# Kernel optimization log

Hardware: AMD Instinct MI355X
Metric: run time of the kernel (lower is better)

The kernel has to match this reference:

```python
import jax, jax.numpy as jnp
import numpy as np

B, T, C = 64, 512, 1024
D = C // 2  # split_len1 == split_len2
CLAMP = 5.0


def e(s):
    # exp(clamp * 0.636 * atan(s / clamp))
    return jnp.exp(CLAMP * 0.636 * jnp.arctan(s / CLAMP))


def gru_cell(x, h, Wih, Whh, bih, bhh):
    # Standard GRU cell, gate order (r, z, n) as in torch.nn.GRUCell.
    gi = x @ Wih.T + bih  # [B, 3D]
    gh = h @ Whh.T + bhh  # [B, 3D]
    i_r, i_z, i_n = gi[:, :D], gi[:, D:2 * D], gi[:, 2 * D:]
    h_r, h_z, h_n = gh[:, :D], gh[:, D:2 * D], gh[:, 2 * D:]
    r = jax.nn.sigmoid(i_r + h_r)
    z = jax.nn.sigmoid(i_z + h_z)
    n = jnp.tanh(i_n + r * h_n)
    return (1.0 - z) * n + z * h


def setup_inputs() -> dict:
    key = jax.random.key(0)
    ks = jax.random.split(key, 20)

    def p(k, shape, scale=0.05):
        return jax.random.normal(k, shape, jnp.float32) * scale

    inp = {"x": jax.random.normal(ks[0], (B, T, C), jnp.float32)}
    for i, name in enumerate(["s1", "s2"]):
        b = 1 + i * 6
        inp[f"{name}_Wih"] = p(ks[b], (3 * D, D))
        inp[f"{name}_Whh"] = p(ks[b + 1], (3 * D, D))
        inp[f"{name}_bih"] = p(ks[b + 2], (3 * D,))
        inp[f"{name}_bhh"] = p(ks[b + 3], (3 * D,))
        inp[f"{name}_Wo"] = p(ks[b + 4], (2 * D, D))
        inp[f"{name}_bo"] = p(ks[b + 5], (2 * D,))
    inp["cg1_W"] = p(ks[13], (D, D))
    inp["cg1_b"] = p(ks[14], (D,))
    inp["cg2_W"] = p(ks[15], (D, D))
    inp["cg2_b"] = p(ks[16], (D,))
    return inp


def reference(x, s1_Wih, s1_Whh, s1_bih, s1_bhh, s1_Wo, s1_bo,
              s2_Wih, s2_Whh, s2_bih, s2_bhh, s2_Wo, s2_bo,
              cg1_W, cg1_b, cg2_W, cg2_b):
    batch = x.shape[0]

    def step(carry, xt):
        h1, h2 = carry
        x1, x2 = xt[:, :D], xt[:, D:]
        # s2 GRU block on x2
        h2n = gru_cell(x2, h2, s2_Wih, s2_Whh, s2_bih, s2_bhh)
        r2 = h2n @ s2_Wo.T + s2_bo
        s2v, t2 = r2[:, :D], r2[:, D:]
        y1 = e(s2v) * x1 + t2
        # gate x2 with cg1 of OLD h1
        x2g = x2 * e(h1 @ cg1_W.T + cg1_b)
        # s1 GRU block on y1
        h1n = gru_cell(y1, h1, s1_Wih, s1_Whh, s1_bih, s1_bhh)
        r1 = h1n @ s1_Wo.T + s1_bo
        s1v, t1 = r1[:, :D], r1[:, D:]
        y2 = e(s1v) * x2g + t1
        # gate y1 with cg2 of OLD h2
        y1o = y1 * e(h2 @ cg2_W.T + cg2_b)
        return (h1n, h2n), jnp.concatenate([y1o, y2], axis=1)

    h0 = (jnp.zeros((batch, D), x.dtype), jnp.zeros((batch, D), x.dtype))
    _, ys = jax.lax.scan(step, h0, jnp.swapaxes(x, 0, 1))  # [T, B, C]
    return jnp.swapaxes(ys, 0, 1)  # [B, T, C]
```

## Files before the change

kernel.cpp:

```cpp
#include <hip/hip_runtime.h>
#include <math.h>

constexpr int kT = 512;
constexpr int kC = 1024;
constexpr int kD = 512;

typedef __attribute__((ext_vector_type(8))) short bf16x8;
typedef __attribute__((ext_vector_type(4))) float f32x4;
typedef __attribute__((ext_vector_type(4))) unsigned int u32x4;

__device__ __forceinline__ float b2f(unsigned short u) {
  unsigned int v = ((unsigned int)u) << 16;
  return __builtin_bit_cast(float, v);
}
__device__ __forceinline__ unsigned short f2b(float f) {
  unsigned int u = __builtin_bit_cast(unsigned int, f);
  u += 0x7fffu + ((u >> 16) & 1u);
  return (unsigned short)(u >> 16);
}
__device__ __forceinline__ float sigm(float x) {
  x = fminf(15.f, fmaxf(-15.f, x));
  return 1.f / (1.f + __expf(-x));
}
__device__ __forceinline__ float tanh_(float x) {
  x = fminf(15.f, fmaxf(-15.f, x));
  float e2 = __expf(2.f * x);
  return (e2 - 1.f) / (e2 + 1.f);
}
__device__ __forceinline__ float efun(float s) {
  return __expf((5.0f * 0.636f) * atanf(s * 0.2f));
}

__device__ __forceinline__ void st_b16_wt(unsigned short* p, unsigned short v) {
  asm volatile("global_store_short %0, %1, off sc0 sc1" ::"v"(p),
               "v"((unsigned int)v)
               : "memory");
}
__device__ __forceinline__ void st_f32_wt(float* p, float v) {
  asm volatile("global_store_dword %0, %1, off sc0 sc1" ::"v"(p), "v"(v)
               : "memory");
}

__device__ __forceinline__ unsigned int ldflag(const unsigned int* p) {
  return __hip_atomic_load(p, __ATOMIC_RELAXED, __HIP_MEMORY_SCOPE_AGENT);
}

__global__ __launch_bounds__(256) void cvt_x2_kernel(
    const float* __restrict__ x, unsigned short* __restrict__ xb2) {
  const int idx = blockIdx.x * 256 + threadIdx.x;
  const int e = idx * 8;
  const int dd = e & 511;
  const int tb = e >> 9;
  const int b = tb & 63;
  const int t = tb >> 6;
  const float* src = x + ((size_t)b * kT + t) * kC + kD + dd;
  f32x4 v0 = *(const f32x4*)src;
  f32x4 v1 = *(const f32x4*)(src + 4);
  bf16x8 o;
#pragma unroll
  for (int j = 0; j < 4; j++) {
    o[j] = (short)f2b(v0[j]);
    o[j + 4] = (short)f2b(v1[j]);
  }
  *(bf16x8*)(xb2 + e) = o;
}

__global__ __launch_bounds__(256, 1) void fused_glow_kernel(
    const float* __restrict__ x, const unsigned short* __restrict__ xb2,
    const float* __restrict__ A_Wih, const float* __restrict__ A_Whh,
    const float* __restrict__ A_bih, const float* __restrict__ A_bhh,
    const float* __restrict__ A_Wo, const float* __restrict__ A_bo,
    const float* __restrict__ A_cgW, const float* __restrict__ A_cgb,
    const float* __restrict__ B_Wih, const float* __restrict__ B_Whh,
    const float* __restrict__ B_bih, const float* __restrict__ B_bhh,
    const float* __restrict__ B_Wo, const float* __restrict__ B_bo,
    const float* __restrict__ B_cgW, const float* __restrict__ B_cgb,
    unsigned short* __restrict__ y1buf, float* __restrict__ out,
    unsigned short* __restrict__ hbA, unsigned short* __restrict__ hbB,
    unsigned int* __restrict__ flagsA, unsigned int* __restrict__ flagsB) {
  const int g = blockIdx.x;
  const bool isA = (g < 64);
  const int gl = isA ? g : (g - 64);
  const int tid = threadIdx.x;
  const int w = tid >> 6;
  const int l = tid & 63;
  const int q = l & 15;
  const int kg = l >> 4;
  const bool lo = (q < 8);
  const int qm = q & 7;
  const int d = 8 * gl + qm;
  const int browbase = 16 * w + 4 * kg;
  const int arow = 16 * w + q;
  const int acol = kg * 8;

  const float* Wih = isA ? A_Wih : B_Wih;
  const float* Whh = isA ? A_Whh : B_Whh;
  const float* bih = isA ? A_bih : B_bih;
  const float* bhh = isA ? A_bhh : B_bhh;
  const float* Wo = isA ? A_Wo : B_Wo;
  const float* bo = isA ? A_bo : B_bo;
  const float* cgW = isA ? A_cgW : B_cgW;
  const float* cgb = isA ? A_cgb : B_cgb;
  unsigned short* hbuf = isA ? hbA : hbB;
  unsigned int* myflag = (isA ? flagsA : flagsB) + (size_t)w * 64 + gl;
  const unsigned int* pollA = flagsA + (size_t)w * 64;
  const unsigned int* pollB = flagsB + (size_t)w * 64;

  __shared__ __attribute__((aligned(16))) unsigned short wlds[80 * 512];
  for (int c = tid; c < 80 * 64; c += 256) {
    const int u = c >> 6, kb = c & 63;
    const int s8 = 8 * gl + (u & 7);
    const int sel = u >> 3;
    u32x4 v = {0u, 0u, 0u, 0u};
    if (sel < 9) {
      const float* wrp = (sel == 0)   ? Whh + (size_t)s8 * kD
                         : (sel == 1) ? Whh + (size_t)(512 + s8) * kD
                         : (sel == 2) ? Whh + (size_t)(1024 + s8) * kD
                         : (sel == 3) ? cgW + (size_t)s8 * kD
                         : (sel == 4) ? Wo + (size_t)s8 * kD
                         : (sel == 5) ? Wo + (size_t)(512 + s8) * kD
                         : (sel == 6) ? Wih + (size_t)s8 * kD
                         : (sel == 7) ? Wih + (size_t)(512 + s8) * kD
                                      : Wih + (size_t)(1024 + s8) * kD;
      const float* p = wrp + kb * 8;
#pragma unroll
      for (int j = 0; j < 4; j++)
        v[j] = (unsigned int)f2b(p[2 * j]) | ((unsigned int)f2b(p[2 * j + 1]) << 16);
    }
    const int byteoff = u * 1024 + ((kb * 16) ^ ((u & 15) << 4));
    *(u32x4*)((char*)wlds + byteoff) = v;
  }

  float biasv[5];
  biasv[0] = lo ? bhh[d] : bhh[512 + d];
  biasv[1] = lo ? bhh[1024 + d] : cgb[d];
  biasv[2] = lo ? bo[d] : bo[512 + d];
  biasv[3] = lo ? bih[d] : bih[512 + d];
  biasv[4] = lo ? bih[1024 + d] : 0.f;

  float hsl[4] = {0.f, 0.f, 0.f, 0.f};
  float ecp[4];
#pragma unroll
  for (int r = 0; r < 4; r++) ecp[r] = efun(cgb[d]);

  __syncthreads();

  const int sw = q << 4;
  const int s0 = isA ? 0 : 2;
  const int s1 = isA ? 512 : 514;
#pragma unroll 1
  for (int s = s0; s <= s1; ++s) {
    const int it = isA ? s : (s - 2);

    bf16x8 ax[16];
    float xopf[4] = {0.f, 0.f, 0.f, 0.f};
    if (isA) {
      const int itc = it < 511 ? it : 511;
      const unsigned short* xp = xb2 + ((size_t)itc * 64 + arow) * 512 + acol;
#pragma unroll
      for (int kk = 0; kk < 16; kk++) ax[kk] = *(const bf16x8*)(xp + kk * 32);
      if (lo) {
        const int ttc = s >= 1 ? s - 1 : 0;
#pragma unroll
        for (int r = 0; r < 4; r++)
          xopf[r] = x[(size_t)(browbase + r) * (kT * kC) + (size_t)ttc * kC + d];
      }
      if (s >= 1) {
        const unsigned int* fp = pollA + l;
        unsigned int v = ldflag(fp);
        while (!__all((int)(v >= (unsigned)s))) {
          __builtin_amdgcn_s_sleep(1);
          v = ldflag(fp);
        }
      }
    } else {
      if (lo) {
        const int ttc = it >= 1 ? it - 1 : 0;
#pragma unroll
        for (int r = 0; r < 4; r++)
          xopf[r] =
              x[(size_t)(browbase + r) * (kT * kC) + (size_t)ttc * kC + kD + d];
      }
      {
        const unsigned int tgtA = (unsigned)(s <= 513 ? s : 513);
        const unsigned int* fp = pollA + l;
        unsigned int v = ldflag(fp);
        while (!__all((int)(v >= tgtA))) {
          __builtin_amdgcn_s_sleep(1);
          v = ldflag(fp);
        }
      }
      const int ity = it < 511 ? it : 511;
      const unsigned short* yp = y1buf + ((size_t)ity * 64 + arow) * 512 + acol;
#pragma unroll
      for (int kk = 0; kk < 16; kk++) ax[kk] = *(const bf16x8*)(yp + kk * 32);
      if (s >= 3) {
        const unsigned int* fp = pollB + l;
        unsigned int v = ldflag(fp);
        while (!__all((int)(v >= (unsigned)s))) {
          __builtin_amdgcn_s_sleep(1);
          v = ldflag(fp);
        }
      }
    }

    const unsigned short* hp =
        hbuf + (size_t)(isA ? s : it) * 32768 + (size_t)arow * 512 + acol;
    bf16x8 ah[16];
#pragma unroll
    for (int kk = 0; kk < 16; kk++) ah[kk] = *(const bf16x8*)(hp + kk * 32);

    f32x4 acc0 = {0.f, 0.f, 0.f, 0.f}, acc1 = {0.f, 0.f, 0.f, 0.f};
    f32x4 acc2 = {0.f, 0.f, 0.f, 0.f}, acc3 = {0.f, 0.f, 0.f, 0.f};
    f32x4 acc4 = {0.f, 0.f, 0.f, 0.f};
#pragma unroll
    for (int kk = 0; kk < 16; kk++) {
      const int kbyte = (kk * 32 + kg * 8) * 2;
      bf16x8 b0 = *(const bf16x8*)((const char*)wlds + q * 1024 + (kbyte ^ sw));
      bf16x8 b1 =
          *(const bf16x8*)((const char*)wlds + (16 + q) * 1024 + (kbyte ^ sw));
      bf16x8 b2 =
          *(const bf16x8*)((const char*)wlds + (32 + q) * 1024 + (kbyte ^ sw));
      bf16x8 b3 =
          *(const bf16x8*)((const char*)wlds + (48 + q) * 1024 + (kbyte ^ sw));
      bf16x8 b4 =
          *(const bf16x8*)((const char*)wlds + (64 + q) * 1024 + (kbyte ^ sw));
      acc0 = __builtin_amdgcn_mfma_f32_16x16x32_bf16(ah[kk], b0, acc0, 0, 0, 0);
      acc1 = __builtin_amdgcn_mfma_f32_16x16x32_bf16(ah[kk], b1, acc1, 0, 0, 0);
      acc2 = __builtin_amdgcn_mfma_f32_16x16x32_bf16(ah[kk], b2, acc2, 0, 0, 0);
      acc3 = __builtin_amdgcn_mfma_f32_16x16x32_bf16(ax[kk], b3, acc3, 0, 0, 0);
      acc4 = __builtin_amdgcn_mfma_f32_16x16x32_bf16(ax[kk], b4, acc4, 0, 0, 0);
    }
    float ab0[4], ab1[4], ab2[4], ab3[4], ab4[4];
#pragma unroll
    for (int r = 0; r < 4; r++) {
      ab0[r] = acc0[r] + biasv[0];
      ab1[r] = acc1[r] + biasv[1];
      ab2[r] = acc2[r] + biasv[2];
      ab3[r] = acc3[r] + biasv[3];
      ab4[r] = acc4[r] + biasv[4];
    }
    float ghz[4], tv[4], giz[4], ec_sh[4];
#pragma unroll
    for (int r = 0; r < 4; r++) {
      ghz[r] = __shfl_xor(ab0[r], 8, 64);
      tv[r] = __shfl_xor(ab2[r], 8, 64);
      giz[r] = __shfl_xor(ab3[r], 8, 64);
      ec_sh[r] = __shfl_xor(ecp[r], 8, 64);
    }

    const int tt = it - 1;
    float yvs[4] = {0.f, 0.f, 0.f, 0.f};
    if (lo) {
#pragma unroll
      for (int r = 0; r < 4; r++) {
        const int b = browbase + r;
        if (isA && it >= 1) {
          yvs[r] = efun(ab2[r]) * xopf[r] + tv[r];
          st_b16_wt(y1buf + ((size_t)tt * 64 + b) * 512 + d, f2b(yvs[r]));
        }
        if (it <= 511) {
          const float rr = sigm(ab3[r] + ab0[r]);
          const float zz = sigm(giz[r] + ghz[r]);
          const float nn = tanh_(ab4[r] + rr * ab1[r]);
          const float hn = (1.f - zz) * nn + zz * hsl[r];
          hsl[r] = hn;
          st_b16_wt(hbuf + (size_t)(it + 1) * 32768 + (size_t)b * 512 + d,
                    f2b(hn));
        }
      }
    } else {
#pragma unroll
      for (int r = 0; r < 4; r++) ecp[r] = efun(ab1[r]);
    }

    asm volatile("s_waitcnt vmcnt(0)" ::: "memory");
    if (l == 0)
      __hip_atomic_store(myflag, (unsigned)(s + 1), __ATOMIC_RELAXED,
                         __HIP_MEMORY_SCOPE_AGENT);

    if (lo && it >= 1) {
#pragma unroll
      for (int r = 0; r < 4; r++) {
        const int b = browbase + r;
        float* op =
            out + (size_t)b * (kT * kC) + (size_t)tt * kC + (isA ? 0 : kD) + d;
        if (isA) {
          st_f32_wt(op, yvs[r] * ec_sh[r]);
        } else {
          st_f32_wt(op, efun(ab2[r]) * (xopf[r] * ec_sh[r]) + tv[r]);
        }
      }
    }
  }
}

extern "C" void kernel_launch(void* const* d_in, const int* in_sizes, int n_in,
                              void* d_out, int out_size, void* d_ws, size_t ws_size,
                              hipStream_t stream) {
  (void)in_sizes; (void)n_in; (void)out_size; (void)ws_size;
  const float* x = (const float*)d_in[0];
  const float* s1_Wih = (const float*)d_in[1];
  const float* s1_Whh = (const float*)d_in[2];
  const float* s1_bih = (const float*)d_in[3];
  const float* s1_bhh = (const float*)d_in[4];
  const float* s1_Wo = (const float*)d_in[5];
  const float* s1_bo = (const float*)d_in[6];
  const float* s2_Wih = (const float*)d_in[7];
  const float* s2_Whh = (const float*)d_in[8];
  const float* s2_bih = (const float*)d_in[9];
  const float* s2_bhh = (const float*)d_in[10];
  const float* s2_Wo = (const float*)d_in[11];
  const float* s2_bo = (const float*)d_in[12];
  const float* cg1_W = (const float*)d_in[13];
  const float* cg1_b = (const float*)d_in[14];
  const float* cg2_W = (const float*)d_in[15];
  const float* cg2_b = (const float*)d_in[16];
  float* out = (float*)d_out;
  char* ws = (char*)d_ws;

  unsigned short* xb2 = (unsigned short*)ws;
  unsigned short* y1b = (unsigned short*)(ws + 33554432);
  unsigned short* hbA = (unsigned short*)(ws + 67108864);
  unsigned short* hbB = (unsigned short*)(ws + 100728832);
  unsigned int* flagsA = (unsigned int*)(ws + 134348800);
  unsigned int* flagsB = (unsigned int*)(ws + 134348800 + 4096);

  hipMemsetAsync(ws + 67108864, 0, 65536, stream);
  hipMemsetAsync(ws + 100728832, 0, 65536, stream);
  hipMemsetAsync(ws + 134348800, 0, 8192, stream);

  cvt_x2_kernel<<<8192, 256, 0, stream>>>(x, xb2);

  fused_glow_kernel<<<128, 256, 0, stream>>>(
      x, xb2,
      s2_Wih, s2_Whh, s2_bih, s2_bhh, s2_Wo, s2_bo, cg2_W, cg2_b,
      s1_Wih, s1_Whh, s1_bih, s1_bhh, s1_Wo, s1_bo, cg1_W, cg1_b,
      y1b, out, hbA, hbB, flagsA, flagsB);
}
```

Measured before the change: 3.664 ms.

## Co-locate both GRU chains in one 512-thread block per column slice

The A and B recurrent chains now share a single 512-thread workgroup per 8-column slice, so the grid drops from 128 to 64 blocks. Both weight sets are staged together in a larger LDS buffer of 144 rows, and the fifth weight tile is trimmed to 8 live rows with its own swizzle instead of zero padding. Cross-chain data can then be exchanged on the same CU, and fewer CUs take part in the global flag spin-waits. In exchange each block uses twice the LDS and threads, and both chains now compete for one CU's MFMA and memory bandwidth.

```diff
diff --git a/kernel.cpp b/kernel.cpp
--- a/kernel.cpp
+++ b/kernel.cpp
@@ -65,7 +65,7 @@
   *(bf16x8*)(xb2 + e) = o;
 }
 
-__global__ __launch_bounds__(256, 1) void fused_glow_kernel(
+__global__ __launch_bounds__(512, 1) void fused_glow_kernel(
     const float* __restrict__ x, const unsigned short* __restrict__ xb2,
     const float* __restrict__ A_Wih, const float* __restrict__ A_Whh,
     const float* __restrict__ A_bih, const float* __restrict__ A_bhh,
@@ -78,11 +78,10 @@
     unsigned short* __restrict__ y1buf, float* __restrict__ out,
     unsigned short* __restrict__ hbA, unsigned short* __restrict__ hbB,
     unsigned int* __restrict__ flagsA, unsigned int* __restrict__ flagsB) {
-  const int g = blockIdx.x;
-  const bool isA = (g < 64);
-  const int gl = isA ? g : (g - 64);
+  const int gl = blockIdx.x;
   const int tid = threadIdx.x;
-  const int w = tid >> 6;
+  const bool isA = (tid < 256);
+  const int w = (tid >> 6) & 3;
   const int l = tid & 63;
   const int q = l & 15;
   const int kg = l >> 4;
@@ -93,41 +92,41 @@
   const int arow = 16 * w + q;
   const int acol = kg * 8;
 
-  const float* Wih = isA ? A_Wih : B_Wih;
-  const float* Whh = isA ? A_Whh : B_Whh;
   const float* bih = isA ? A_bih : B_bih;
   const float* bhh = isA ? A_bhh : B_bhh;
-  const float* Wo = isA ? A_Wo : B_Wo;
   const float* bo = isA ? A_bo : B_bo;
-  const float* cgW = isA ? A_cgW : B_cgW;
   const float* cgb = isA ? A_cgb : B_cgb;
   unsigned short* hbuf = isA ? hbA : hbB;
   unsigned int* myflag = (isA ? flagsA : flagsB) + (size_t)w * 64 + gl;
   const unsigned int* pollA = flagsA + (size_t)w * 64;
   const unsigned int* pollB = flagsB + (size_t)w * 64;
 
-  __shared__ __attribute__((aligned(16))) unsigned short wlds[80 * 512];
-  for (int c = tid; c < 80 * 64; c += 256) {
+  __shared__ __attribute__((aligned(16))) unsigned short wlds[144 * 512];
+  for (int c = tid; c < 144 * 64; c += 512) {
     const int u = c >> 6, kb = c & 63;
-    const int s8 = 8 * gl + (u & 7);
-    const int sel = u >> 3;
-    u32x4 v = {0u, 0u, 0u, 0u};
-    if (sel < 9) {
-      const float* wrp = (sel == 0)   ? Whh + (size_t)s8 * kD
-                         : (sel == 1) ? Whh + (size_t)(512 + s8) * kD
-                         : (sel == 2) ? Whh + (size_t)(1024 + s8) * kD
-                         : (sel == 3) ? cgW + (size_t)s8 * kD
-                         : (sel == 4) ? Wo + (size_t)s8 * kD
-                         : (sel == 5) ? Wo + (size_t)(512 + s8) * kD
-                         : (sel == 6) ? Wih + (size_t)s8 * kD
-                         : (sel == 7) ? Wih + (size_t)(512 + s8) * kD
-                                      : Wih + (size_t)(1024 + s8) * kD;
-      const float* p = wrp + kb * 8;
-#pragma unroll
-      for (int j = 0; j < 4; j++)
-        v[j] = (unsigned int)f2b(p[2 * j]) | ((unsigned int)f2b(p[2 * j + 1]) << 16);
-    }
-    const int byteoff = u * 1024 + ((kb * 16) ^ ((u & 15) << 4));
+    const int ch = u / 72;
+    const int ur = u - ch * 72;
+    const int sel = ur >> 3;
+    const int s8 = 8 * gl + (ur & 7);
+    const float* Whh_ = ch ? B_Whh : A_Whh;
+    const float* Wih_ = ch ? B_Wih : A_Wih;
+    const float* Wo_ = ch ? B_Wo : A_Wo;
+    const float* cgW_ = ch ? B_cgW : A_cgW;
+    const float* wrp = (sel == 0)   ? Whh_ + (size_t)s8 * kD
+                       : (sel == 1) ? Whh_ + (size_t)(512 + s8) * kD
+                       : (sel == 2) ? Whh_ + (size_t)(1024 + s8) * kD
+                       : (sel == 3) ? cgW_ + (size_t)s8 * kD
+                       : (sel == 4) ? Wo_ + (size_t)s8 * kD
+                       : (sel == 5) ? Wo_ + (size_t)(512 + s8) * kD
+                       : (sel == 6) ? Wih_ + (size_t)s8 * kD
+                       : (sel == 7) ? Wih_ + (size_t)(512 + s8) * kD
+                                    : Wih_ + (size_t)(1024 + s8) * kD;
+    const float* p = wrp + kb * 8;
+    u32x4 v;
+#pragma unroll
+    for (int j = 0; j < 4; j++)
+      v[j] = (unsigned int)f2b(p[2 * j]) | ((unsigned int)f2b(p[2 * j + 1]) << 16);
+    const int byteoff = (ch * 72 + ur) * 1024 + ((kb * 16) ^ ((ur & 15) << 4));
     *(u32x4*)((char*)wlds + byteoff) = v;
   }
 
@@ -145,7 +144,9 @@
 
   __syncthreads();
 
+  const char* wb = (const char*)wlds + (isA ? 0 : 73728);
   const int sw = q << 4;
+  const int sw4 = qm << 4;
   const int s0 = isA ? 0 : 2;
   const int s1 = isA ? 512 : 514;
 #pragma unroll 1
@@ -216,15 +217,11 @@
 #pragma unroll
     for (int kk = 0; kk < 16; kk++) {
       const int kbyte = (kk * 32 + kg * 8) * 2;
-      bf16x8 b0 = *(const bf16x8*)((const char*)wlds + q * 1024 + (kbyte ^ sw));
-      bf16x8 b1 =
-          *(const bf16x8*)((const char*)wlds + (16 + q) * 1024 + (kbyte ^ sw));
-      bf16x8 b2 =
-          *(const bf16x8*)((const char*)wlds + (32 + q) * 1024 + (kbyte ^ sw));
-      bf16x8 b3 =
-          *(const bf16x8*)((const char*)wlds + (48 + q) * 1024 + (kbyte ^ sw));
-      bf16x8 b4 =
-          *(const bf16x8*)((const char*)wlds + (64 + q) * 1024 + (kbyte ^ sw));
+      bf16x8 b0 = *(const bf16x8*)(wb + q * 1024 + (kbyte ^ sw));
+      bf16x8 b1 = *(const bf16x8*)(wb + (16 + q) * 1024 + (kbyte ^ sw));
+      bf16x8 b2 = *(const bf16x8*)(wb + (32 + q) * 1024 + (kbyte ^ sw));
+      bf16x8 b3 = *(const bf16x8*)(wb + (48 + q) * 1024 + (kbyte ^ sw));
+      bf16x8 b4 = *(const bf16x8*)(wb + (64 + qm) * 1024 + (kbyte ^ sw4));
       acc0 = __builtin_amdgcn_mfma_f32_16x16x32_bf16(ah[kk], b0, acc0, 0, 0, 0);
       acc1 = __builtin_amdgcn_mfma_f32_16x16x32_bf16(ah[kk], b1, acc1, 0, 0, 0);
       acc2 = __builtin_amdgcn_mfma_f32_16x16x32_bf16(ah[kk], b2, acc2, 0, 0, 0);
@@ -332,7 +329,7 @@
 
   cvt_x2_kernel<<<8192, 256, 0, stream>>>(x, xb2);
 
-  fused_glow_kernel<<<128, 256, 0, stream>>>(
+  fused_glow_kernel<<<64, 512, 0, stream>>>(
       x, xb2,
       s2_Wih, s2_Whh, s2_bih, s2_bhh, s2_Wo, s2_bo, cg2_W, cg2_b,
       s1_Wih, s1_Whh, s1_bih, s1_bhh, s1_Wo, s1_bo, cg1_W, cg1_b,
```

Result: slower. 4.840 ms (+32.1%).
